# Performance work log

Hardware: AMD Instinct MI355X
Metric: run time of the kernel (lower is better)

## Reference

```python
import jax, jax.numpy as jnp
import numpy as np

EMBED_DIM = 1024
NUM_HEADS = 16
SEQ_LEN = 2048
BATCH = 2
LN_EPS = 1e-5


def setup_inputs() -> dict:
    key = jax.random.key(0)
    ks = jax.random.split(key, 12)
    d = EMBED_DIM
    s = 1.0 / np.sqrt(d)
    inp = {
        "x": jax.random.normal(ks[0], (BATCH, SEQ_LEN, d), dtype=jnp.float32),
        "ln1_g": jnp.ones((d,), jnp.float32),
        "ln1_b": jnp.zeros((d,), jnp.float32),
        "ln2_g": jnp.ones((d,), jnp.float32),
        "ln2_b": jnp.zeros((d,), jnp.float32),
        "W_qkv": jax.random.normal(ks[1], (d, 3 * d), jnp.float32) * s,
        "b_qkv": jnp.zeros((3 * d,), jnp.float32),
        "W_proj": jax.random.normal(ks[2], (d, d), jnp.float32) * s,
        "b_proj": jnp.zeros((d,), jnp.float32),
        "W_fc": jax.random.normal(ks[3], (d, 4 * d), jnp.float32) * s,
        "b_fc": jnp.zeros((4 * d,), jnp.float32),
        "W_out": jax.random.normal(ks[4], (4 * d, d), jnpp_dummy := jnp.float32) * (1.0 / np.sqrt(4 * d)),
        "b_out": jnp.zeros((d,), jnp.float32),
    }
    return inp


def _layernorm(x, g, b):
    mu = jnp.mean(x, axis=-1, keepdims=True)
    var = jnp.mean(jnp.square(x - mu), axis=-1, keepdims=True)
    return (x - mu) * jax.lax.rsqrt(var + LN_EPS) * g + b


def _block(x, ln1_g, ln1_b, ln2_g, ln2_b, W_qkv, b_qkv, W_proj, b_proj, W_fc, b_fc, W_out, b_out):
    B, S, D = x.shape
    H = NUM_HEADS
    hd = D // H
    h = _layernorm(x, ln1_g, ln1_b)
    qkv = h @ W_qkv + b_qkv  # [B,S,3D]
    q, k, v = jnp.split(qkv, 3, axis=-1)
    # [B,H,S,hd]
    q = q.reshape(B, S, H, hd).transpose(0, 2, 1, 3)
    k = k.reshape(B, S, H, hd).transpose(0, 2, 1, 3)
    v = v.reshape(B, S, H, hd).transpose(0, 2, 1, 3)
    attn = jnp.einsum("bhqd,bhkd->bhqk", q, k) / np.sqrt(hd).astype(np.float32)
    causal = jnp.tril(jnp.ones((S, S), dtype=bool))
    attn = jnp.where(causal, attn, -jnp.inf)
    attn = jax.nn.softmax(attn, axis=-1)
    y = jnp.einsum("bhqk,bhkd->bhqd", attn, v)
    y = y.transpose(0, 2, 1, 3).reshape(B, S, D)
    y = y @ W_proj + b_proj
    x = x + y
    h2 = _layernorm(x, ln2_g, ln2_b)
    m = jax.nn.relu(h2 @ W_fc + b_fc) @ W_out + b_out
    return x + m


def reference(x, ln1_g, ln1_b, ln2_g, ln2_b, W_qkv, b_qkv, W_proj, b_proj, W_fc, b_fc, W_out, b_out):
    return _block(x, ln1_g, ln1_b, ln2_g, ln2_b, W_qkv, b_qkv, W_proj, b_proj, W_fc, b_fc, W_out, b_out)
```

## Files before the change

### kernel.cpp

```cpp
#include <hip/hip_runtime.h>

typedef unsigned short u16;
typedef __attribute__((ext_vector_type(8))) __bf16 bf16x8;
typedef __attribute__((ext_vector_type(4))) float f32x4;

#define DEV __device__ __forceinline__

DEV u16 f2bf(float f) {
  unsigned u = __float_as_uint(f);
  u += 0x7fffu + ((u >> 16) & 1u);
  return (u16)(u >> 16);
}
DEV float bf2f(u16 u) { return __uint_as_float((unsigned)u << 16); }

DEV void gl_lds16(const void* g, void* l) {
  __builtin_amdgcn_global_load_lds(
      (const __attribute__((address_space(1))) void*)(uintptr_t)g,
      (__attribute__((address_space(3))) void*)(unsigned)(uintptr_t)l, 16, 0, 0);
}

DEV float wave_sum64(float v) {
#pragma unroll
  for (int off = 32; off > 0; off >>= 1) v += __shfl_down(v, off);
  return v;
}

DEV void ln_body(const float4 v, const float* g, const float* be, u16* out_row, int t,
                 float* red) {
  const int w = t >> 6, L = t & 63;
  float s = v.x + v.y + v.z + v.w;
  s = wave_sum64(s);
  if (L == 0) red[w] = s;
  __syncthreads();
  const float mean = (red[0] + red[1] + red[2] + red[3]) * (1.0f / 1024.0f);
  const float dx = v.x - mean, dy = v.y - mean, dz = v.z - mean, dw = v.w - mean;
  float q = dx * dx + dy * dy + dz * dz + dw * dw;
  q = wave_sum64(q);
  if (L == 0) red[4 + w] = q;
  __syncthreads();
  const float var = (red[4] + red[5] + red[6] + red[7]) * (1.0f / 1024.0f);
  const float rs = rsqrtf(var + 1e-5f);
  const float4 gg = reinterpret_cast<const float4*>(g)[t];
  const float4 bb = reinterpret_cast<const float4*>(be)[t];
  ushort4 o;
  o.x = f2bf(dx * rs * gg.x + bb.x);
  o.y = f2bf(dy * rs * gg.y + bb.y);
  o.z = f2bf(dz * rs * gg.z + bb.z);
  o.w = f2bf(dw * rs * gg.w + bb.w);
  reinterpret_cast<ushort4*>(out_row)[t] = o;
}

__global__ __launch_bounds__(256) void prep_kernel(
    const float* __restrict__ x, const float* __restrict__ ln1g,
    const float* __restrict__ ln1b, u16* __restrict__ hbuf,
    const float* __restrict__ Wqkv, u16* __restrict__ wt_qkv,
    const float* __restrict__ Wproj, u16* __restrict__ wt_proj,
    const float* __restrict__ Wfc, u16* __restrict__ wt_fc,
    const float* __restrict__ Wout, u16* __restrict__ wt_out) {
  __shared__ float smem[32 * 33];
  int id = blockIdx.x;
  const int t = threadIdx.x;
  if (id < 4096) {
    const float4 v = reinterpret_cast<const float4*>(x + (size_t)id * 1024)[t];
    ln_body(v, ln1g, ln1b, hbuf + (size_t)id * 1024, t, smem);
    return;
  }
  id -= 4096;
  const float* W;
  u16* Wt;
  int K, N, nbx;
  if (id < 3072) {
    W = Wqkv; Wt = wt_qkv; K = 1024; N = 3072; nbx = 96;
  } else if (id < 3072 + 1024) {
    id -= 3072; W = Wproj; Wt = wt_proj; K = 1024; N = 1024; nbx = 32;
  } else if (id < 3072 + 1024 + 4096) {
    id -= 3072 + 1024; W = Wfc; Wt = wt_fc; K = 1024; N = 4096; nbx = 128;
  } else {
    id -= 3072 + 1024 + 4096; W = Wout; Wt = wt_out; K = 4096; N = 1024; nbx = 32;
  }
  float(*tile)[33] = (float(*)[33])smem;
  const int c0 = (id % nbx) * 32, r0 = (id / nbx) * 32;
  const int tx = t & 31, ty = t >> 5;
#pragma unroll
  for (int j = 0; j < 4; ++j)
    tile[ty + j * 8][tx] = W[(size_t)(r0 + ty + j * 8) * N + c0 + tx];
  __syncthreads();
#pragma unroll
  for (int j = 0; j < 4; ++j) {
    const int n = c0 + ty + j * 8, k = r0 + tx;
    Wt[(size_t)n * K + k] = f2bf(tile[tx][ty + j * 8]);
  }
}

__global__ __launch_bounds__(256) void proj_reduce_ln(const float* __restrict__ x,
                                                      const float* __restrict__ bias,
                                                      const u16* __restrict__ P0,
                                                      const u16* __restrict__ P1,
                                                      const float* __restrict__ g,
                                                      const float* __restrict__ be,
                                                      float* __restrict__ x2,
                                                      u16* __restrict__ hbuf) {
  const int row = blockIdx.x, t = threadIdx.x;
  const size_t off = (size_t)row * 1024;
  __shared__ float red[8];
  const float4 xv = reinterpret_cast<const float4*>(x + off)[t];
  const float4 bv = reinterpret_cast<const float4*>(bias)[t];
  const ushort4 p0 = reinterpret_cast<const ushort4*>(P0 + off)[t];
  const ushort4 p1 = reinterpret_cast<const ushort4*>(P1 + off)[t];
  float4 v;
  v.x = xv.x + bv.x + bf2f(p0.x) + bf2f(p1.x);
  v.y = xv.y + bv.y + bf2f(p0.y) + bf2f(p1.y);
  v.z = xv.z + bv.z + bf2f(p0.z) + bf2f(p1.z);
  v.w = xv.w + bv.w + bf2f(p0.w) + bf2f(p1.w);
  reinterpret_cast<float4*>(x2 + off)[t] = v;
  ln_body(v, g, be, hbuf + off, t, red);
}

__global__ __launch_bounds__(256) void out_reduce(const float* __restrict__ x2,
                                                  const float* __restrict__ bias,
                                                  const u16* __restrict__ P0,
                                                  const u16* __restrict__ P1,
                                                  const u16* __restrict__ P2,
                                                  const u16* __restrict__ P3,
                                                  float* __restrict__ dout) {
  const int row = blockIdx.x, t = threadIdx.x;
  const size_t off = (size_t)row * 1024;
  const float4 xv = reinterpret_cast<const float4*>(x2 + off)[t];
  const float4 bv = reinterpret_cast<const float4*>(bias)[t];
  const ushort4 a = reinterpret_cast<const ushort4*>(P0 + off)[t];
  const ushort4 b = reinterpret_cast<const ushort4*>(P1 + off)[t];
  const ushort4 c = reinterpret_cast<const ushort4*>(P2 + off)[t];
  const ushort4 d = reinterpret_cast<const ushort4*>(P3 + off)[t];
  float4 o;
  o.x = xv.x + bv.x + bf2f(a.x) + bf2f(b.x) + bf2f(c.x) + bf2f(d.x);
  o.y = xv.y + bv.y + bf2f(a.y) + bf2f(b.y) + bf2f(c.y) + bf2f(d.y);
  o.z = xv.z + bv.z + bf2f(a.z) + bf2f(b.z) + bf2f(c.z) + bf2f(d.z);
  o.w = xv.w + bv.w + bf2f(a.w) + bf2f(b.w) + bf2f(c.w) + bf2f(d.w);
  reinterpret_cast<float4*>(dout + off)[t] = o;
}

enum { F_BIAS = 1, F_RESID = 2, F_RELU = 4, F_BF16 = 8, F_PART4 = 32, F_VT = 64 };

template <int FLAGS>
__global__ __launch_bounds__(256, 2) void gemm_bt(const u16* __restrict__ A,
                                                  const u16* __restrict__ Bt,
                                                  const float* __restrict__ bias,
                                                  const float* __restrict__ resid,
                                                  void* __restrict__ Cout,
                                                  u16* __restrict__ pp0, u16* __restrict__ pp1,
                                                  u16* __restrict__ pp2, u16* __restrict__ pp3,
                                                  int M, int N, int K, int Kst) {
  __shared__ __attribute__((aligned(16))) u16 sA[2][128 * 32];
  __shared__ __attribute__((aligned(16))) u16 sB[2][128 * 32];

  const int gx = gridDim.x, gy = gridDim.y;
  const int tilesPerZ = gx * gy;
  int lin = (blockIdx.z * gy + blockIdx.y) * gx + blockIdx.x;
  const int total = tilesPerZ * gridDim.z;
  if (!(total & 7)) lin = (lin & 7) * (total >> 3) + (lin >> 3);
  const int zz = lin / tilesPerZ;
  const int pid = lin - zz * tilesPerZ;
  const int npg = gx << 3;
  const int gid = pid / npg;
  const int rem = pid - gid * npg;
  const int fm = gid << 3;
  const int gsm = (gy - fm < 8) ? (gy - fm) : 8;
  const int bm = fm + rem % gsm;
  const int bn = rem / gsm;

  const int t = threadIdx.x, w = t >> 6, L = t & 63, quad = L >> 4, l15 = L & 15;
  const int wm = w >> 1, wn = w & 1;
  const int m0 = bm * 128, n0 = bn * 128;
  const u16* Ag = A + (size_t)m0 * Kst + (size_t)zz * K;
  const u16* Bg = Bt + (size_t)n0 * Kst + (size_t)zz * K;

  f32x4 acc[4][4] = {};

  for (int k0 = 0; k0 < K; k0 += 64) {
    __syncthreads();
#pragma unroll
    for (int h = 0; h < 2; ++h) {
#pragma unroll
      for (int i = 0; i < 2; ++i) {
        const int cp = i * 256 + t, rr = cp >> 2, cc = (cp & 3) << 3;
        gl_lds16(Ag + (size_t)rr * Kst + k0 + h * 32 + cc, &sA[h][(i * 256 + w * 64) * 8]);
      }
#pragma unroll
      for (int i = 0; i < 2; ++i) {
        const int cp = i * 256 + t, rr = cp >> 2, cc = (cp & 3) << 3;
        gl_lds16(Bg + (size_t)rr * Kst + k0 + h * 32 + cc, &sB[h][(i * 256 + w * 64) * 8]);
      }
    }
    __syncthreads();

#pragma unroll
    for (int h = 0; h < 2; ++h) {
      bf16x8 af[4], bfr[4];
#pragma unroll
      for (int m = 0; m < 4; ++m)
        af[m] = *(const bf16x8*)&sA[h][(wm * 64 + m * 16 + l15) * 32 + quad * 8];
#pragma unroll
      for (int n = 0; n < 4; ++n)
        bfr[n] = *(const bf16x8*)&sB[h][(wn * 64 + n * 16 + l15) * 32 + quad * 8];
#pragma unroll
      for (int m = 0; m < 4; ++m)
#pragma unroll
        for (int n = 0; n < 4; ++n)
          acc[m][n] =
              __builtin_amdgcn_mfma_f32_16x16x32_bf16(af[m], bfr[n], acc[m][n], 0, 0, 0);
    }
  }

  if ((FLAGS & F_VT) && n0 >= 2048) {
#pragma unroll
    for (int m = 0; m < 4; ++m) {
#pragma unroll
      for (int n = 0; n < 4; ++n) {
        const int col = n0 + wn * 64 + n * 16 + l15;
        const float bv = bias[col];
        const int hh = (col - 2048) >> 6, dd = col & 63;
        const int srow = m0 + wm * 64 + m * 16 + quad * 4;
        const int bb = srow >> 11, ss = srow & 2047;
        ushort4 tmp;
        tmp.x = f2bf(acc[m][n][0] + bv);
        tmp.y = f2bf(acc[m][n][1] + bv);
        tmp.z = f2bf(acc[m][n][2] + bv);
        tmp.w = f2bf(acc[m][n][3] + bv);
        *(ushort4*)(pp0 + ((size_t)((bb * 16 + hh) * 64 + dd)) * 2048 + ss) = tmp;
      }
    }
    return;
  }

  u16* pbase = nullptr;
  if (FLAGS & F_PART4)
    pbase = (zz == 0) ? pp0 : (zz == 1) ? pp1 : (zz == 2) ? pp2 : pp3;

#pragma unroll
  for (int m = 0; m < 4; ++m) {
#pragma unroll
    for (int n = 0; n < 4; ++n) {
      const int col = n0 + wn * 64 + n * 16 + l15;
      const float bv = (FLAGS & F_BIAS) ? bias[col] : 0.0f;
#pragma unroll
      for (int rr = 0; rr < 4; ++rr) {
        const int row = m0 + wm * 64 + m * 16 + quad * 4 + rr;
        if (FLAGS & F_PART4) {
          pbase[(size_t)row * N + col] = f2bf(acc[m][n][rr]);
        } else {
          float v = acc[m][n][rr] + bv;
          if (FLAGS & F_RESID) v += resid[(size_t)row * N + col];
          if (FLAGS & F_RELU) v = fmaxf(v, 0.0f);
          if (FLAGS & F_BF16)
            ((u16*)Cout)[(size_t)row * N + col] = f2bf(v);
          else
            ((float*)Cout)[(size_t)row * N + col] = v;
        }
      }
    }
  }
}

__global__ __launch_bounds__(256) void flash_attn(const u16* __restrict__ qkv,
                                                  const u16* __restrict__ Vt,
                                                  u16* __restrict__ y,
                                                  float* __restrict__ acc0,
                                                  float* __restrict__ acc1,
                                                  float* __restrict__ lacc0,
                                                  float* __restrict__ lacc1) {
  constexpr int S = 2048, D3 = 3072, D = 1024;
  constexpr float Csc = 0.125f * 1.44269504088896f;
  __shared__ __attribute__((aligned(16))) u16 sK[64 * 64];
  __shared__ __attribute__((aligned(16))) u16 sV[64 * 64];
  __shared__ __attribute__((aligned(16))) u16 sP[4][2 * 16 * 40];

  const int bid = blockIdx.x;
  const int bh = bid & 31;
  const int e = bid >> 5;
  int qt, it0, it1, part;
  if (e < 16) {
    qt = 16 + e; it0 = 0; it1 = 16; part = 1;
  } else {
    const int j = (e - 16) >> 1;
    if (((e - 16) & 1) == 0) {
      qt = 15 - j; it0 = 0; it1 = qt + 1; part = 0;
    } else {
      qt = 31 - j; it0 = 16; it1 = qt + 1; part = 2;
    }
  }
  const int b = bh >> 4, h = bh & 15;
  const int q0 = qt * 64;

  const int t = threadIdx.x, w = t >> 6, L = t & 63, quad = L >> 4, l15 = L & 15;
  const int qw = q0 + w * 16;

  const u16* qbase = qkv + (size_t)(b * S) * D3 + h * 64;
  const u16* Kbase = qbase + D;
  const u16* Vbase = Vt + (size_t)((b * 16 + h) * 64) * S;

  const u16* Ksrc[2];
  const u16* Vsrc[2];
#pragma unroll
  for (int i = 0; i < 2; ++i) {
    const int p = i * 256 + t;
    const int row = p >> 3;
    const int k8 = ((p & 7) ^ (row & 7)) << 3;
    Ksrc[i] = Kbase + (size_t)row * D3 + k8;
    Vsrc[i] = Vbase + (size_t)row * S + k8;
  }

  bf16x8 aQ[2];
#pragma unroll
  for (int kk = 0; kk < 2; ++kk)
    aQ[kk] = *(const bf16x8*)(qbase + (size_t)(qw + l15) * D3 + kk * 32 + quad * 8);

  bf16x8 ones;
#pragma unroll
  for (int i = 0; i < 8; ++i) ones[i] = (__bf16)1.0f;

  f32x4 acc[4] = {};
  f32x4 lacc = {};

  u16* sPw = sP[w];
  const int swz = l15 & 7;

  {
    const int kv0 = it0 * 64;
#pragma unroll
    for (int i = 0; i < 2; ++i)
      gl_lds16(Ksrc[i] + (size_t)kv0 * D3, &sK[(i * 256 + w * 64) * 8]);
#pragma unroll
    for (int i = 0; i < 2; ++i)
      gl_lds16(Vsrc[i] + kv0, &sV[(i * 256 + w * 64) * 8]);
  }

  for (int it = it0; it < it1; ++it) {
    const int kv0 = it * 64;
    asm volatile("s_waitcnt vmcnt(0)" ::: "memory");
    __builtin_amdgcn_s_barrier();

    f32x4 s[4] = {};
#pragma unroll
    for (int kk = 0; kk < 2; ++kk) {
#pragma unroll
      for (int n = 0; n < 4; ++n) {
        const bf16x8 bK =
            *(const bf16x8*)&sK[(n * 16 + l15) * 64 + ((kk * 4 + quad) ^ swz) * 8];
        s[n] = __builtin_amdgcn_mfma_f32_16x16x32_bf16(aQ[kk], bK, s[n], 0, 0, 0);
      }
    }

    if (kv0 + 63 > qw) {
#pragma unroll
      for (int n = 0; n < 4; ++n) {
        const int col = kv0 + n * 16 + l15;
#pragma unroll
        for (int r = 0; r < 4; ++r) {
          const int row = qw + quad * 4 + r;
          const float p = __builtin_amdgcn_exp2f(s[n][r] * Csc);
          s[n][r] = (col > row) ? 0.0f : p;
        }
      }
    } else {
#pragma unroll
      for (int n = 0; n < 4; ++n)
#pragma unroll
        for (int r = 0; r < 4; ++r) s[n][r] = __builtin_amdgcn_exp2f(s[n][r] * Csc);
    }

#pragma unroll
    for (int n = 0; n < 4; ++n)
#pragma unroll
      for (int r = 0; r < 4; ++r)
        sPw[(n >> 1) * 640 + (quad * 4 + r) * 40 + (n & 1) * 16 + l15] = f2bf(s[n][r]);

#pragma unroll
    for (int kk = 0; kk < 2; ++kk) {
      const bf16x8 aP = *(const bf16x8*)&sPw[kk * 640 + l15 * 40 + quad * 8];
      lacc = __builtin_amdgcn_mfma_f32_16x16x32_bf16(aP, ones, lacc, 0, 0, 0);
#pragma unroll
      for (int dn = 0; dn < 4; ++dn) {
        const bf16x8 bV =
            *(const bf16x8*)&sV[(dn * 16 + l15) * 64 + ((kk * 4 + quad) ^ swz) * 8];
        acc[dn] = __builtin_amdgcn_mfma_f32_16x16x32_bf16(aP, bV, acc[dn], 0, 0, 0);
      }
    }

    asm volatile("s_waitcnt lgkmcnt(0)" ::: "memory");
    __builtin_amdgcn_s_barrier();
    if (it + 1 < it1) {
      const int kvn = kv0 + 64;
#pragma unroll
      for (int i = 0; i < 2; ++i)
        gl_lds16(Ksrc[i] + (size_t)kvn * D3, &sK[(i * 256 + w * 64) * 8]);
#pragma unroll
      for (int i = 0; i < 2; ++i)
        gl_lds16(Vsrc[i] + kvn, &sV[(i * 256 + w * 64) * 8]);
    }
  }

  if (part == 0) {
#pragma unroll
    for (int r = 0; r < 4; ++r) {
      const float inv = 1.0f / lacc[r];
      const int row = qw + quad * 4 + r;
      u16* yb = y + (size_t)(b * S + row) * D + h * 64 + l15;
#pragma unroll
      for (int dn = 0; dn < 4; ++dn) yb[dn * 16] = f2bf(acc[dn][r] * inv);
    }
  } else {
    float* accP = (part == 1) ? acc0 : acc1;
    float* laccP = (part == 1) ? lacc0 : lacc1;
#pragma unroll
    for (int r = 0; r < 4; ++r) {
      const int row = qw + quad * 4 + r;
      const int g = (bh << 10) + (row - 1024);
      float* ap = accP + (size_t)g * 64 + l15;
#pragma unroll
      for (int dn = 0; dn < 4; ++dn) ap[dn * 16] = acc[dn][r];
      if (l15 == 0) laccP[g] = lacc[r];
    }
  }
}

__global__ __launch_bounds__(256) void attn_combine(const float* __restrict__ acc0,
                                                    const float* __restrict__ acc1,
                                                    const float* __restrict__ lacc0,
                                                    const float* __restrict__ lacc1,
                                                    u16* __restrict__ y) {
  const int t = threadIdx.x;
  const int g = blockIdx.x * 4 + (t >> 6);
  const int d = t & 63;
  const int bh = g >> 10, ri = g & 1023;
  const int b = bh >> 4, h = bh & 15;
  const int row = 1024 + ri;
  const size_t po = (size_t)g * 64 + d;
  const float l = lacc0[g] + lacc1[g];
  const float v = (acc0[po] + acc1[po]) / l;
  y[((size_t)(b * 2048 + row)) * 1024 + h * 64 + d] = f2bf(v);
}

extern "C" void kernel_launch(void* const* d_in, const int* in_sizes, int n_in,
                              void* d_out, int out_size, void* d_ws, size_t ws_size,
                              hipStream_t stream) {
  const float* x = (const float*)d_in[0];
  const float* ln1g = (const float*)d_in[1];
  const float* ln1b = (const float*)d_in[2];
  const float* ln2g = (const float*)d_in[3];
  const float* ln2b = (const float*)d_in[4];
  const float* Wqkv = (const float*)d_in[5];
  const float* bqkv = (const float*)d_in[6];
  const float* Wproj = (const float*)d_in[7];
  const float* bproj = (const float*)d_in[8];
  const float* Wfc = (const float*)d_in[9];
  const float* bfc = (const float*)d_in[10];
  const float* Wout = (const float*)d_in[11];
  const float* bout = (const float*)d_in[12];

  char* ws = (char*)d_ws;
  const size_t MB = 1u << 20;
  u16* wt_out = (u16*)(ws + 0 * MB);
  u16* hbuf = (u16*)(ws + 8 * MB);
  float* x2 = (float*)(ws + 16 * MB);
  u16* ybuf = (u16*)(ws + 32 * MB);
  u16* qkvb = (u16*)(ws + 40 * MB);
  u16* vtb = (u16*)(ws + 64 * MB);
  u16* wt_qkv = (u16*)(ws + 72 * MB);
  u16* wt_proj = (u16*)(ws + 78 * MB);
  u16* wt_fc = (u16*)(ws + 80 * MB);
  u16* projP0 = (u16*)(ws + 40 * MB);
  u16* projP1 = (u16*)(ws + 48 * MB);
  u16* m1 = (u16*)(ws + 40 * MB);
  u16* po0 = (u16*)(ws + 8 * MB);
  u16* po1 = (u16*)(ws + 32 * MB);
  u16* po2 = (u16*)(ws + 72 * MB);
  u16* po3 = (u16*)(ws + 80 * MB);
  float* facc0 = (float*)(ws + 8 * MB);
  float* facc1 = (float*)(ws + 16 * MB);
  float* flacc0 = (float*)(ws + 24 * MB);
  float* flacc1 = (float*)(ws + 25 * MB);

  prep_kernel<<<4096 + 3072 + 1024 + 4096 + 4096, 256, 0, stream>>>(
      x, ln1g, ln1b, hbuf, Wqkv, wt_qkv, Wproj, wt_proj, Wfc, wt_fc, Wout, wt_out);

  gemm_bt<F_BIAS | F_BF16 | F_VT><<<dim3(24, 32), 256, 0, stream>>>(
      hbuf, wt_qkv, bqkv, nullptr, qkvb, vtb, nullptr, nullptr, nullptr,
      4096, 3072, 1024, 1024);
  flash_attn<<<1536, 256, 0, stream>>>(qkvb, vtb, ybuf, facc0, facc1, flacc0, flacc1);
  attn_combine<<<8192, 256, 0, stream>>>(facc0, facc1, flacc0, flacc1, ybuf);

  gemm_bt<F_PART4><<<dim3(8, 32, 2), 256, 0, stream>>>(
      ybuf, wt_proj, nullptr, nullptr, nullptr, projP0, projP1, nullptr, nullptr,
      4096, 1024, 512, 1024);
  proj_reduce_ln<<<4096, 256, 0, stream>>>(x, bproj, projP0, projP1, ln2g, ln2b, x2, hbuf);

  gemm_bt<F_BIAS | F_RELU | F_BF16><<<dim3(32, 32), 256, 0, stream>>>(
      hbuf, wt_fc, bfc, nullptr, m1, nullptr, nullptr, nullptr, nullptr,
      4096, 4096, 1024, 1024);

  gemm_bt<F_PART4><<<dim3(8, 32, 4), 256, 0, stream>>>(
      m1, wt_out, nullptr, nullptr, nullptr, po0, po1, po2, po3,
      4096, 1024, 1024, 4096);
  out_reduce<<<4096, 256, 0, stream>>>(x2, bout, po0, po1, po2, po3, (float*)d_out);
}
```

Baseline: 319.7 us.

## Use 128-row query tiles with 8 waves in flash attention, add MFMA priority

```diff
diff --git a/kernel.cpp b/kernel.cpp
--- a/kernel.cpp
+++ b/kernel.cpp
@@ -261,7 +261,7 @@
   }
 }
 
-__global__ __launch_bounds__(256) void flash_attn(const u16* __restrict__ qkv,
+__global__ __launch_bounds__(512) void flash_attn(const u16* __restrict__ qkv,
                                                   const u16* __restrict__ Vt,
                                                   u16* __restrict__ y,
                                                   float* __restrict__ acc0,
@@ -272,24 +272,24 @@
   constexpr float Csc = 0.125f * 1.44269504088896f;
   __shared__ __attribute__((aligned(16))) u16 sK[64 * 64];
   __shared__ __attribute__((aligned(16))) u16 sV[64 * 64];
-  __shared__ __attribute__((aligned(16))) u16 sP[4][2 * 16 * 40];
+  __shared__ __attribute__((aligned(16))) u16 sP[8][2 * 16 * 40];
 
   const int bid = blockIdx.x;
   const int bh = bid & 31;
   const int e = bid >> 5;
   int qt, it0, it1, part;
-  if (e < 16) {
-    qt = 16 + e; it0 = 0; it1 = 16; part = 1;
+  if (e < 8) {
+    qt = 8 + e; it0 = 0; it1 = 16; part = 1;
   } else {
-    const int j = (e - 16) >> 1;
-    if (((e - 16) & 1) == 0) {
-      qt = 15 - j; it0 = 0; it1 = qt + 1; part = 0;
+    const int j = (e - 8) >> 1;
+    if (((e - 8) & 1) == 0) {
+      qt = 7 - j; it0 = 0; it1 = 2 * qt + 2; part = 0;
     } else {
-      qt = 31 - j; it0 = 16; it1 = qt + 1; part = 2;
+      qt = 15 - j; it0 = 16; it1 = 2 * qt + 2; part = 2;
     }
   }
   const int b = bh >> 4, h = bh & 15;
-  const int q0 = qt * 64;
+  const int q0 = qt * 128;
 
   const int t = threadIdx.x, w = t >> 6, L = t & 63, quad = L >> 4, l15 = L & 15;
   const int qw = q0 + w * 16;
@@ -298,16 +298,12 @@
   const u16* Kbase = qbase + D;
   const u16* Vbase = Vt + (size_t)((b * 16 + h) * 64) * S;
 
-  const u16* Ksrc[2];
-  const u16* Vsrc[2];
-#pragma unroll
-  for (int i = 0; i < 2; ++i) {
-    const int p = i * 256 + t;
-    const int row = p >> 3;
-    const int k8 = ((p & 7) ^ (row & 7)) << 3;
-    Ksrc[i] = Kbase + (size_t)row * D3 + k8;
-    Vsrc[i] = Vbase + (size_t)row * S + k8;
-  }
+  const int srow = t >> 3;
+  const int k8 = ((t & 7) ^ (srow & 7)) << 3;
+  const u16* Ksrc = Kbase + (size_t)srow * D3 + k8;
+  const u16* Vsrc = Vbase + (size_t)srow * S + k8;
+  u16* sKdst = &sK[(w * 64) * 8];
+  u16* sVdst = &sV[(w * 64) * 8];
 
   bf16x8 aQ[2];
 #pragma unroll
@@ -324,15 +320,8 @@
   u16* sPw = sP[w];
   const int swz = l15 & 7;
 
-  {
-    const int kv0 = it0 * 64;
-#pragma unroll
-    for (int i = 0; i < 2; ++i)
-      gl_lds16(Ksrc[i] + (size_t)kv0 * D3, &sK[(i * 256 + w * 64) * 8]);
-#pragma unroll
-    for (int i = 0; i < 2; ++i)
-      gl_lds16(Vsrc[i] + kv0, &sV[(i * 256 + w * 64) * 8]);
-  }
+  gl_lds16(Ksrc + (size_t)(it0 * 64) * D3, sKdst);
+  gl_lds16(Vsrc + it0 * 64, sVdst);
 
   for (int it = it0; it < it1; ++it) {
     const int kv0 = it * 64;
@@ -340,6 +329,7 @@
     __builtin_amdgcn_s_barrier();
 
     f32x4 s[4] = {};
+    __builtin_amdgcn_s_setprio(1);
 #pragma unroll
     for (int kk = 0; kk < 2; ++kk) {
 #pragma unroll
@@ -349,6 +339,7 @@
         s[n] = __builtin_amdgcn_mfma_f32_16x16x32_bf16(aQ[kk], bK, s[n], 0, 0, 0);
       }
     }
+    __builtin_amdgcn_s_setprio(0);
 
     if (kv0 + 63 > qw) {
 #pragma unroll
@@ -374,6 +365,7 @@
       for (int r = 0; r < 4; ++r)
         sPw[(n >> 1) * 640 + (quad * 4 + r) * 40 + (n & 1) * 16 + l15] = f2bf(s[n][r]);
 
+    __builtin_amdgcn_s_setprio(1);
 #pragma unroll
     for (int kk = 0; kk < 2; ++kk) {
       const bf16x8 aP = *(const bf16x8*)&sPw[kk * 640 + l15 * 40 + quad * 8];
@@ -385,17 +377,14 @@
         acc[dn] = __builtin_amdgcn_mfma_f32_16x16x32_bf16(aP, bV, acc[dn], 0, 0, 0);
       }
     }
+    __builtin_amdgcn_s_setprio(0);
 
     asm volatile("s_waitcnt lgkmcnt(0)" ::: "memory");
     __builtin_amdgcn_s_barrier();
     if (it + 1 < it1) {
       const int kvn = kv0 + 64;
-#pragma unroll
-      for (int i = 0; i < 2; ++i)
-        gl_lds16(Ksrc[i] + (size_t)kvn * D3, &sK[(i * 256 + w * 64) * 8]);
-#pragma unroll
-      for (int i = 0; i < 2; ++i)
-        gl_lds16(Vsrc[i] + kvn, &sV[(i * 256 + w * 64) * 8]);
+      gl_lds16(Ksrc + (size_t)kvn * D3, sKdst);
+      gl_lds16(Vsrc + kvn, sVdst);
     }
   }
 
@@ -486,7 +475,7 @@
   gemm_bt<F_BIAS | F_BF16 | F_VT><<<dim3(24, 32), 256, 0, stream>>>(
       hbuf, wt_qkv, bqkv, nullptr, qkvb, vtb, nullptr, nullptr, nullptr,
       4096, 3072, 1024, 1024);
-  flash_attn<<<1536, 256, 0, stream>>>(qkvb, vtb, ybuf, facc0, facc1, flacc0, flacc1);
+  flash_attn<<<768, 512, 0, stream>>>(qkvb, vtb, ybuf, facc0, facc1, flacc0, flacc1);
   attn_combine<<<8192, 256, 0, stream>>>(facc0, facc1, flacc0, flacc1, ybuf);
 
   gemm_bt<F_PART4><<<dim3(8, 32, 2), 256, 0, stream>>>(
```

After: 315.1 us. Within noise of the previous version (-1.4%).
